# Performance work log

Measured on AMD Instinct MI355X. Metric: run time of the kernel, lower is better.

## Reference

```python
import jax, jax.numpy as jnp
import numpy as np

N = 50000   # nodes
E = 800000  # edges (avg degree 16)
D = 128     # in_dim = out_dim
H = 8       # heads
O = D // H  # per-head dim = 16
FF = 512    # ffn inner hidden
LN_EPS = 1e-6
LRELU_SLOPE = 0.01  # torch F.leaky_relu default


def setup_inputs() -> dict:
    key = jax.random.key(0)
    ks = jax.random.split(key, 9)
    x = jax.random.normal(ks[0], (N, D), jnp.float32)
    src = jax.random.randint(ks[1], (E,), 0, N)
    dst = jax.random.randint(ks[2], (E,), 0, N)
    fc_w = jax.random.normal(ks[3], (H, D, O), jnp.float32) * 0.05
    a_l = jax.random.normal(ks[4], (H, O), jnp.float32) * 0.05
    a_r = jax.random.normal(ks[5], (H, O), jnp.float32) * 0.05
    w1 = jax.random.normal(ks[6], (D, FF), jnp.float32) * 0.05
    b1 = jnp.zeros((FF,), jnp.float32)
    w2 = jax.random.normal(ks[7], (FF, D), jnp.float32) * 0.05
    b2 = jnp.zeros((D,), jnp.float32)
    ln_g = jnp.ones((D,), jnp.float32)
    ln_b = jnp.zeros((D,), jnp.float32)
    return dict(x=x, fc_w=fc_w, a_l=a_l, a_r=a_r, ln_g=ln_g, ln_b=ln_b,
                w1=w1, b1=b1, w2=w2, b2=b2, src=src, dst=dst)


def _gat_s2s(x, fc_w, a_l, a_r, src, dst):
    # per-head projection: [N,H,O]
    z = jnp.einsum('nd,hdo->nho', x, fc_w)
    # attn_fc([z_src||z_dst]) == a_l . z_src + a_r . z_dst  (decomposed, same math)
    el = jnp.einsum('nho,ho->nh', z, a_l)  # [N,H]
    er = jnp.einsum('nho,ho->nh', z, a_r)  # [N,H]
    e = jax.nn.leaky_relu(el[src] + er[dst], LRELU_SLOPE)  # [E,H]
    # edge softmax over incoming edges of each dst node (numerically stable)
    m = jax.ops.segment_max(e, dst, num_segments=N)  # [N,H]
    m = jnp.where(jnp.isfinite(m), m, 0.0)
    ex = jnp.exp(e - m[dst])  # [E,H]
    denom = jax.ops.segment_sum(ex, dst, num_segments=N)  # [N,H]
    alpha = ex / denom[dst]  # [E,H]
    # weighted aggregation of source features: [N,H,O]
    agg = jax.ops.segment_sum(alpha[:, :, None] * z[src], dst, num_segments=N)
    return agg.reshape(N, H * O)  # head concat -> [N,D]


def _ffn(h, ln_g, ln_b, w1, b1, w2, b2):
    # pre-LayerNorm positionwise FFN with gelu and residual (dropout off / eval)
    mu = jnp.mean(h, axis=-1, keepdims=True)
    var = jnp.mean((h - mu) ** 2, axis=-1, keepdims=True)
    ln = (h - mu) * jax.lax.rsqrt(var + LN_EPS) * ln_g + ln_b
    inter = jax.nn.gelu(ln @ w1 + b1, approximate=False)
    return inter @ w2 + b2 + h


def reference(x, fc_w, a_l, a_r, ln_g, ln_b, w1, b1, w2, b2, src, dst):
    h = jax.nn.elu(_gat_s2s(x, fc_w, a_l, a_r, src, dst))
    h = h + x  # residual with origin (S2S: origin == neighbor == x)
    return _ffn(h, ln_g, ln_b, w1, b1, w2, b2)
```

## Files before the change

### kernel.cpp

```cpp
#include <hip/hip_runtime.h>

#define NN 50000
#define EE 800000
#define LDK 136
#define SLOTS 64
#define FEPT 8
#define NFA 157
#define SPLITE (NFA * 256 * FEPT)
#define NFB 234
#define CONVB 2048

#define C_X    0
#define C_ZW   6400000
#define C_AL   6416384
#define C_AR   6416512
#define C_LNG  6416640
#define C_LNB  6416768
#define C_W1T  6416896
#define C_B1   6482432
#define C_W2T  6482944
#define C_B2   6548480
#define C_WAT  6548608
#define C_TOT  6550656

typedef __attribute__((ext_vector_type(8))) short bf16x8;
typedef __attribute__((ext_vector_type(4))) float f32x4;

__device__ __forceinline__ float bf2f(unsigned short u) {
  union { unsigned int i; float f; } v; v.i = ((unsigned int)u) << 16; return v.f;
}
__device__ __forceinline__ unsigned short f2bf(float f) {
  union { float f; unsigned int i; } v; v.f = f;
  unsigned int r = v.i + 0x7fffu + ((v.i >> 16) & 1u);
  return (unsigned short)(r >> 16);
}
__device__ __forceinline__ int ld_idx(const void* p, int i, int is64) {
  return is64 ? (int)((const long long*)p)[i] : ((const int*)p)[i];
}

__device__ __forceinline__ float fast_gelu(float u) {
  float ax = fabsf(u) * 0.70710678118654752f;
  float d  = fmaf(0.3275911f, ax, 1.f);
  float r  = __builtin_amdgcn_rcpf(d);
  r = r * fmaf(-d, r, 2.f);
  float p = fmaf(1.061405429f, r, -1.453152027f);
  p = fmaf(p, r, 1.421413741f);
  p = fmaf(p, r, -0.284496736f);
  p = fmaf(p, r, 0.254829592f);
  p = p * r;
  float e = __expf(-ax * ax);
  float erfv = fmaf(-p, e, 1.f);
  union { float f; unsigned int i; } su, se;
  su.f = u; se.f = erfv;
  se.i = se.i | (su.i & 0x80000000u);
  return 0.5f * u * (1.f + se.f);
}

__global__ void k_probe(const unsigned short* __restrict__ xr,
                        const int* __restrict__ s, const int* __restrict__ d,
                        int* __restrict__ flags) {
  int i = blockIdx.x * 256 + threadIdx.x;
  int bad = 0, zc = 0, zs = 0, zd = 0;
  for (int j = i; j < 65536; j += 32 * 256) {
    unsigned short u = xr[j];
    if ((u & 0x7F80u) == 0x7F80u) bad = 1;
    if (((j & 1) == 0) && u == 0) zc++;
  }
  for (int j = i; j < 131072; j += 32 * 256) {
    if (j & 1) {
      if (s[j] == 0) zs++;
      if (d[j] == 0) zd++;
    }
  }
  if (bad) atomicOr(&flags[0], 1);
  if (zc) atomicAdd(&flags[1], zc);
  if (zs) atomicAdd(&flags[2], zs);
  if (zd) atomicAdd(&flags[3], zd);
}

__device__ __forceinline__ void do_fill(const void* __restrict__ src,
                                        const void* __restrict__ dst,
                                        const int* __restrict__ iflags,
                                        int* __restrict__ cnt,
                                        unsigned short* __restrict__ esrc,
                                        int base) {
  if (base >= EE) return;
  const int s64 = iflags[0] > 1000, d64 = iflags[1] > 1000;
  int dv[FEPT], sv[FEPT];
  if (!d64 && base + FEPT <= EE) {
    const int4* p = (const int4*)((const int*)dst + base);
    int4 a = p[0], b = p[1];
    dv[0]=a.x; dv[1]=a.y; dv[2]=a.z; dv[3]=a.w; dv[4]=b.x; dv[5]=b.y; dv[6]=b.z; dv[7]=b.w;
  } else {
#pragma unroll
    for (int j = 0; j < FEPT; j++) dv[j] = (base + j < EE) ? ld_idx(dst, base + j, d64) : 0;
  }
  if (!s64 && base + FEPT <= EE) {
    const int4* p = (const int4*)((const int*)src + base);
    int4 a = p[0], b = p[1];
    sv[0]=a.x; sv[1]=a.y; sv[2]=a.z; sv[3]=a.w; sv[4]=b.x; sv[5]=b.y; sv[6]=b.z; sv[7]=b.w;
  } else {
#pragma unroll
    for (int j = 0; j < FEPT; j++) sv[j] = (base + j < EE) ? ld_idx(src, base + j, s64) : 0;
  }
#pragma unroll
  for (int j = 0; j < FEPT; j++) {
    if (base + j < EE) {
      unsigned d = (unsigned)dv[j]; if (d >= NN) d = 0;
      unsigned s = (unsigned)sv[j]; if (s >= NN) s = 0;
      int p = atomicAdd(&cnt[d], 1);
      if (p < SLOTS) esrc[d * SLOTS + p] = (unsigned short)s;
    }
  }
}

__global__ __launch_bounds__(256) void k_convfill(
    const void* __restrict__ x, const void* __restrict__ fcw,
    const void* __restrict__ a_l, const void* __restrict__ a_r,
    const void* __restrict__ lng, const void* __restrict__ lnb,
    const void* __restrict__ w1, const void* __restrict__ b1,
    const void* __restrict__ w2, const void* __restrict__ b2,
    const int* __restrict__ flags, unsigned short* __restrict__ canon,
    const void* __restrict__ srcp, const void* __restrict__ dstp,
    int* __restrict__ cnt, unsigned short* __restrict__ esrc) {
  if (blockIdx.x < NFA) {
    do_fill(srcp, dstp, flags + 2, cnt, esrc, (blockIdx.x * 256 + threadIdx.x) * FEPT);
    return;
  }
  const int isf32 = (flags[0] != 0) || (flags[1] > 8192);
  const int tid0 = (blockIdx.x - NFA) * 256 + threadIdx.x;
  for (int v = tid0; v < (C_ZW >> 3); v += CONVB * 256) {
    if (isf32) {
      const float* xf = (const float*)x + v * 8;
      float4 a = *(const float4*)xf;
      float4 b = *(const float4*)(xf + 4);
      union { unsigned short u[8]; uint4 q; } pk;
      pk.u[0] = f2bf(a.x); pk.u[1] = f2bf(a.y); pk.u[2] = f2bf(a.z); pk.u[3] = f2bf(a.w);
      pk.u[4] = f2bf(b.x); pk.u[5] = f2bf(b.y); pk.u[6] = f2bf(b.z); pk.u[7] = f2bf(b.w);
      *(uint4*)(canon + v * 8) = pk.q;
    } else {
      *(uint4*)(canon + v * 8) = *(const uint4*)((const unsigned short*)x + v * 8);
    }
  }
  for (int i = C_ZW + tid0; i < C_TOT; i += CONVB * 256) {
    unsigned short v;
    if (i >= C_WAT) {
      int j = i - C_WAT; int c = j >> 7, dd = j & 127; int h = c & 7;
      const void* fa = (c < 8) ? a_l : a_r;
      float s = 0.f;
      if (isf32) {
        const float* fw = (const float*)fcw + h * 2048 + dd * 16;
        const float* fv = (const float*)fa + h * 16;
#pragma unroll
        for (int o = 0; o < 16; o++) s += fw[o] * fv[o];
      } else {
        const unsigned short* fw = (const unsigned short*)fcw + h * 2048 + dd * 16;
        const unsigned short* fv = (const unsigned short*)fa + h * 16;
#pragma unroll
        for (int o = 0; o < 16; o++) s += bf2f(fw[o]) * bf2f(fv[o]);
      }
      v = f2bf(s);
    } else {
      const void* src; int idx;
      if (i < C_AL)       { int j = i - C_ZW; int c = j >> 7, d = j & 127; src = fcw; idx = (c >> 4) * 2048 + d * 16 + (c & 15); }
      else if (i < C_AR)  { src = a_l; idx = i - C_AL; }
      else if (i < C_LNG) { src = a_r; idx = i - C_AR; }
      else if (i < C_LNB) { src = lng; idx = i - C_LNG; }
      else if (i < C_W1T) { src = lnb; idx = i - C_LNB; }
      else if (i < C_B1)  { int j = i - C_W1T; int n = j >> 7, k = j & 127; src = w1; idx = k * 512 + n; }
      else if (i < C_W2T) { src = b1;  idx = i - C_B1; }
      else if (i < C_B2)  { int j = i - C_W2T; int n = j >> 9, k = j & 511; src = w2; idx = k * 128 + n; }
      else                { src = b2;  idx = i - C_B2; }
      if (isf32) v = f2bf(((const float*)src)[idx]);
      else       v = ((const unsigned short*)src)[idx];
    }
    canon[i] = v;
  }
}

__global__ __launch_bounds__(256) void k_projfill(
    const unsigned short* __restrict__ canon,
    unsigned short* __restrict__ z, float* __restrict__ el, float* __restrict__ er,
    const void* __restrict__ srcp, const void* __restrict__ dstp,
    const int* __restrict__ iflags,
    int* __restrict__ cnt, unsigned short* __restrict__ esrc) {
  __shared__ unsigned short sA[128 * LDK];
  __shared__ unsigned short sB[64 * LDK];
  if (blockIdx.x < NFB) {
    do_fill(srcp, dstp, iflags, cnt, esrc,
            SPLITE + (blockIdx.x * 256 + threadIdx.x) * FEPT);
    return;
  }
  const int pid = blockIdx.x - NFB;
  const unsigned short* xc  = canon + C_X;
  const unsigned short* zwt = canon + C_ZW;
  const unsigned short* wat = canon + C_WAT;
  const int tid = threadIdx.x;
  const int row0 = (pid >> 1) * 128;
  const int n0 = (pid & 1) * 64;
  for (int v = tid; v < 2048; v += 256) {
    int r = v >> 4, k8 = (v & 15) << 3;
    int gr = row0 + r; if (gr >= NN) gr = NN - 1;
    *(uint4*)(&sA[r * LDK + k8]) = *(const uint4*)(xc + gr * 128 + k8);
  }
  for (int v = tid; v < 1024; v += 256) {
    int n = v >> 4, k8 = (v & 15) << 3;
    *(uint4*)(&sB[n * LDK + k8]) = *(const uint4*)(zwt + (n0 + n) * 128 + k8);
  }
  __syncthreads();
  const int lane = tid & 63, w = tid >> 6;
  const int mr = lane & 15, q = lane >> 4;
  const f32x4 zero = {0.f, 0.f, 0.f, 0.f};
  f32x4 acc[8];
#pragma unroll
  for (int i = 0; i < 8; i++) acc[i] = zero;
#pragma unroll
  for (int kc = 0; kc < 4; kc++) {
    bf16x8 b = *(const bf16x8*)(&sB[(w * 16 + mr) * LDK + kc * 32 + q * 8]);
#pragma unroll
    for (int mt = 0; mt < 8; mt++) {
      bf16x8 a = *(const bf16x8*)(&sA[(mt * 16 + mr) * LDK + kc * 32 + q * 8]);
      acc[mt] = __builtin_amdgcn_mfma_f32_16x16x32_bf16(a, b, acc[mt], 0, 0, 0);
    }
  }
  const int col = n0 + w * 16 + mr;
#pragma unroll
  for (int mt = 0; mt < 8; mt++) {
#pragma unroll
    for (int r = 0; r < 4; r++) {
      int grow = row0 + mt * 16 + q * 4 + r;
      if (grow < NN) z[grow * 128 + col] = f2bf(acc[mt][r]);
    }
  }
  if (n0 == 0) {
    f32x4 e0 = zero, e1 = zero;
#pragma unroll
    for (int kc = 0; kc < 4; kc++) {
      bf16x8 b = *(const bf16x8*)(wat + mr * 128 + kc * 32 + q * 8);
      bf16x8 a0 = *(const bf16x8*)(&sA[(w * 16 + mr) * LDK + kc * 32 + q * 8]);
      bf16x8 a1 = *(const bf16x8*)(&sA[((w + 4) * 16 + mr) * LDK + kc * 32 + q * 8]);
      e0 = __builtin_amdgcn_mfma_f32_16x16x32_bf16(a0, b, e0, 0, 0, 0);
      e1 = __builtin_amdgcn_mfma_f32_16x16x32_bf16(a1, b, e1, 0, 0, 0);
    }
    float* eo = (mr < 8) ? el : er;
    const int hh = mr & 7;
#pragma unroll
    for (int r = 0; r < 4; r++) {
      int g0 = row0 + w * 16 + q * 4 + r;
      int g1 = row0 + (w + 4) * 16 + q * 4 + r;
      if (g0 < NN) eo[g0 * 8 + hh] = e0[r];
      if (g1 < NN) eo[g1 * 8 + hh] = e1[r];
    }
  }
}

__global__ __launch_bounds__(256) void k_agg(
    const unsigned short* __restrict__ canon, const unsigned short* __restrict__ z,
    const float* __restrict__ el, const float* __restrict__ er,
    const int* __restrict__ cnt, const unsigned short* __restrict__ esrc,
    const void* __restrict__ srcp, const void* __restrict__ dstp,
    const int* __restrict__ iflags,
    float* __restrict__ h1out, float2* __restrict__ mars) {
  const unsigned short* xc = canon + C_X;
  const int lane = threadIdx.x & 63;
  const int node = blockIdx.x * 4 + (threadIdx.x >> 6);
  if (node >= NN) return;
  const int degr = cnt[node];
  const int hl = lane & 7;
  const int g  = lane >> 3;
  const float ern = er[node * 8 + hl];

  float m = -3.0e38f;
  float acc[16];
#pragma unroll
  for (int j = 0; j < 16; j++) acc[j] = 0.f;
  float denom = 0.f;

  if (degr <= SLOTS) {
    const int deg = degr;
    const unsigned short* eptr = esrc + node * SLOTS;
    for (int b = 0; b < deg; b += 16) {
      int e0 = b + g, e1 = b + g + 8;
      int c0 = (e0 < deg) ? e0 : deg - 1;
      int c1 = (e1 < deg) ? e1 : deg - 1;
      unsigned s0 = eptr[c0]; if (s0 >= NN) s0 = 0;
      unsigned s1 = eptr[c1]; if (s1 >= NN) s1 = 0;
      float t0 = el[s0 * 8 + hl] + ern;
      float t1 = el[s1 * 8 + hl] + ern;
      t0 = (t0 > 0.f) ? t0 : 0.01f * t0;
      t1 = (t1 > 0.f) ? t1 : 0.01f * t1;
      if (e0 < deg) m = fmaxf(m, t0);
      if (e1 < deg) m = fmaxf(m, t1);
    }
    m = fmaxf(m, __shfl_xor(m, 8));
    m = fmaxf(m, __shfl_xor(m, 16));
    m = fmaxf(m, __shfl_xor(m, 32));
    for (int b = 0; b < deg; b += 16) {
      int e0 = b + g, e1 = b + g + 8;
      int c0 = (e0 < deg) ? e0 : deg - 1;
      int c1 = (e1 < deg) ? e1 : deg - 1;
      unsigned s0 = eptr[c0]; if (s0 >= NN) s0 = 0;
      unsigned s1 = eptr[c1]; if (s1 >= NN) s1 = 0;
      float t0 = el[s0 * 8 + hl] + ern;
      float t1 = el[s1 * 8 + hl] + ern;
      bf16x8 za0 = *(const bf16x8*)(z + s0 * 128 + hl * 16);
      bf16x8 za1 = *(const bf16x8*)(z + s0 * 128 + hl * 16 + 8);
      bf16x8 zb0 = *(const bf16x8*)(z + s1 * 128 + hl * 16);
      bf16x8 zb1 = *(const bf16x8*)(z + s1 * 128 + hl * 16 + 8);
      t0 = (t0 > 0.f) ? t0 : 0.01f * t0;
      t1 = (t1 > 0.f) ? t1 : 0.01f * t1;
      float ex0 = (e0 < deg) ? __expf(fminf(t0 - m, 0.f)) : 0.f;
      float ex1 = (e1 < deg) ? __expf(fminf(t1 - m, 0.f)) : 0.f;
      denom += ex0 + ex1;
#pragma unroll
      for (int j = 0; j < 8; j++) {
        acc[j]     += ex0 * bf2f((unsigned short)za0[j]) + ex1 * bf2f((unsigned short)zb0[j]);
        acc[j + 8] += ex0 * bf2f((unsigned short)za1[j]) + ex1 * bf2f((unsigned short)zb1[j]);
      }
    }
  } else {
    const int s64 = iflags[0] > 1000, d64 = iflags[1] > 1000;
    for (int b = 0; b < EE; b += 8) {
      int e = b + g;
      unsigned dd = (unsigned)ld_idx(dstp, e, d64); if (dd >= NN) dd = 0;
      bool ok = (dd == (unsigned)node);
      unsigned s0 = (unsigned)ld_idx(srcp, e, s64); if (s0 >= NN) s0 = 0;
      float t0 = el[s0 * 8 + hl] + ern;
      t0 = (t0 > 0.f) ? t0 : 0.01f * t0;
      if (ok) m = fmaxf(m, t0);
    }
    m = fmaxf(m, __shfl_xor(m, 8));
    m = fmaxf(m, __shfl_xor(m, 16));
    m = fmaxf(m, __shfl_xor(m, 32));
    for (int b = 0; b < EE; b += 8) {
      int e = b + g;
      unsigned dd = (unsigned)ld_idx(dstp, e, d64); if (dd >= NN) dd = 0;
      bool ok = (dd == (unsigned)node);
      unsigned s0 = (unsigned)ld_idx(srcp, e, s64); if (s0 >= NN) s0 = 0;
      float t0 = el[s0 * 8 + hl] + ern;
      t0 = (t0 > 0.f) ? t0 : 0.01f * t0;
      float ex0 = ok ? __expf(fminf(t0 - m, 0.f)) : 0.f;
      denom += ex0;
      bf16x8 za0 = *(const bf16x8*)(z + s0 * 128 + hl * 16);
      bf16x8 za1 = *(const bf16x8*)(z + s0 * 128 + hl * 16 + 8);
#pragma unroll
      for (int j = 0; j < 8; j++) {
        acc[j]     += ex0 * bf2f((unsigned short)za0[j]);
        acc[j + 8] += ex0 * bf2f((unsigned short)za1[j]);
      }
    }
  }

  denom += __shfl_xor(denom, 8);
  denom += __shfl_xor(denom, 16);
  denom += __shfl_xor(denom, 32);
  {
    const bool hi1 = (lane & 32) != 0;
#pragma unroll
    for (int j = 0; j < 8; j++) {
      float send = hi1 ? acc[j] : acc[j + 8];
      float recv = __shfl_xor(send, 32);
      float keep = hi1 ? acc[j + 8] : acc[j];
      acc[j] = keep + recv;
    }
    const bool hi2 = (lane & 16) != 0;
#pragma unroll
    for (int j = 0; j < 4; j++) {
      float send = hi2 ? acc[j] : acc[j + 4];
      float recv = __shfl_xor(send, 16);
      float keep = hi2 ? acc[j + 4] : acc[j];
      acc[j] = keep + recv;
    }
    const bool hi3 = (lane & 8) != 0;
#pragma unroll
    for (int j = 0; j < 2; j++) {
      float send = hi3 ? acc[j] : acc[j + 2];
      float recv = __shfl_xor(send, 8);
      float keep = hi3 ? acc[j + 2] : acc[j];
      acc[j] = keep + recv;
    }
  }
  const float inv = (denom > 0.f) ? 1.f / denom : 0.f;
  const int c = hl * 16 + g * 2;
  float r0 = acc[0] * inv;
  float r1 = acc[1] * inv;
  unsigned int xx = *(const unsigned int*)(xc + node * 128 + c);
  float hv0 = ((r0 > 0.f) ? r0 : (__expf(fminf(r0, 0.f)) - 1.f)) + bf2f((unsigned short)(xx & 0xffffu));
  float hv1 = ((r1 > 0.f) ? r1 : (__expf(fminf(r1, 0.f)) - 1.f)) + bf2f((unsigned short)(xx >> 16));
  float s1 = hv0 + hv1;
  float s2 = hv0 * hv0 + hv1 * hv1;
#pragma unroll
  for (int off = 1; off < 64; off <<= 1) {
    s1 += __shfl_xor(s1, off);
    s2 += __shfl_xor(s2, off);
  }
  if (lane == 0) {
    float mu = s1 * (1.f / 128.f);
    float var = s2 * (1.f / 128.f) - mu * mu;
    mars[node] = make_float2(mu, rsqrtf(fmaxf(var, 0.f) + 1e-6f));
  }
  *(float2*)(h1out + node * 128 + c) = make_float2(hv0, hv1);
}

__global__ __launch_bounds__(512) void k_ffn(
    const unsigned short* __restrict__ canon, const float2* __restrict__ mars,
    float* __restrict__ out) {
  const unsigned short* lngc = canon + C_LNG;
  const unsigned short* lnbc = canon + C_LNB;
  const unsigned short* w1t  = canon + C_W1T;
  const unsigned short* b1c  = canon + C_B1;
  const unsigned short* w2t  = canon + C_W2T;
  const unsigned short* b2c  = canon + C_B2;
  __shared__ unsigned short sLn[64 * LDK];
  __shared__ unsigned short sInt[64 * LDK];
  const int tid = threadIdx.x;
  const int row0 = blockIdx.x * 64;
  {
    const int r = tid >> 3, t8 = tid & 7;
    const int grow = row0 + r;
    const int gr = (grow < NN) ? grow : NN - 1;
    const float2 ms = mars[gr];
    const float* hrow = out + (size_t)gr * 128 + t8 * 16;
#pragma unroll
    for (int h8 = 0; h8 < 2; h8++) {
      float4 a = *(const float4*)(hrow + h8 * 8);
      float4 b = *(const float4*)(hrow + h8 * 8 + 4);
      union { unsigned short u[8]; uint4 q; } gv, bv, pk;
      gv.q = *(const uint4*)(lngc + t8 * 16 + h8 * 8);
      bv.q = *(const uint4*)(lnbc + t8 * 16 + h8 * 8);
      float vv[8] = {a.x, a.y, a.z, a.w, b.x, b.y, b.z, b.w};
#pragma unroll
      for (int j = 0; j < 8; j++)
        pk.u[j] = f2bf((vv[j] - ms.x) * ms.y * bf2f(gv.u[j]) + bf2f(bv.u[j]));
      *(uint4*)(&sLn[r * LDK + t8 * 16 + h8 * 8]) = pk.q;
    }
  }
  __syncthreads();
  const int lane = tid & 63, w = tid >> 6;
  const int mr = lane & 15, q = lane >> 4;
  const f32x4 zero = {0.f, 0.f, 0.f, 0.f};
  f32x4 acc2[4];
#pragma unroll
  for (int a = 0; a < 4; a++) acc2[a] = zero;
#pragma unroll
  for (int qr = 0; qr < 4; qr++) {
    if (qr) __syncthreads();
    const int colg = qr * 128 + w * 16;
    f32x4 a1[4];
#pragma unroll
    for (int a = 0; a < 4; a++) a1[a] = zero;
#pragma unroll
    for (int kc = 0; kc < 4; kc++) {
      bf16x8 wf = *(const bf16x8*)(w1t + (colg + mr) * 128 + kc * 32 + q * 8);
#pragma unroll
      for (int rt = 0; rt < 4; rt++) {
        bf16x8 lf = *(const bf16x8*)(&sLn[(rt * 16 + mr) * LDK + kc * 32 + q * 8]);
        a1[rt] = __builtin_amdgcn_mfma_f32_16x16x32_bf16(wf, lf, a1[rt], 0, 0, 0);
      }
    }
    union { unsigned short u[4]; uint2 v; } b1v;
    b1v.v = *(const uint2*)(b1c + colg + q * 4);
#pragma unroll
    for (int rt = 0; rt < 4; rt++) {
      union { unsigned short u[4]; uint2 v; } pk;
#pragma unroll
      for (int r = 0; r < 4; r++)
        pk.u[r] = f2bf(fast_gelu(a1[rt][r] + bf2f(b1v.u[r])));
      *(uint2*)(&sInt[(rt * 16 + mr) * LDK + w * 16 + q * 4]) = pk.v;
    }
    __syncthreads();
#pragma unroll
    for (int ks = 0; ks < 4; ks++) {
      bf16x8 bw = *(const bf16x8*)(w2t + (w * 16 + mr) * 512 + qr * 128 + ks * 32 + q * 8);
#pragma unroll
      for (int mt = 0; mt < 4; mt++) {
        bf16x8 af = *(const bf16x8*)(&sInt[(mt * 16 + mr) * LDK + ks * 32 + q * 8]);
        acc2[mt] = __builtin_amdgcn_mfma_f32_16x16x32_bf16(af, bw, acc2[mt], 0, 0, 0);
      }
    }
  }
  {
    const int col = w * 16 + mr;
    const float bias = bf2f(b2c[col]);
#pragma unroll
    for (int mt = 0; mt < 4; mt++)
#pragma unroll
      for (int r = 0; r < 4; r++) {
        int grow = row0 + mt * 16 + q * 4 + r;
        if (grow < NN) {
          size_t o = (size_t)grow * 128 + col;
          out[o] = acc2[mt][r] + bias + out[o];
        }
      }
  }
}

extern "C" void kernel_launch(void* const* d_in, const int* in_sizes, int n_in,
                              void* d_out, int out_size, void* d_ws, size_t ws_size,
                              hipStream_t stream) {
  const void* x   = d_in[0];
  const void* fcw = d_in[1];
  const void* a_l = d_in[2];
  const void* a_r = d_in[3];
  const void* lng = d_in[4];
  const void* lnb = d_in[5];
  const void* w1  = d_in[6];
  const void* b1  = d_in[7];
  const void* w2  = d_in[8];
  const void* b2  = d_in[9];
  const void* src = d_in[10];
  const void* dst = d_in[11];
  float* out = (float*)d_out;

  char* ws = (char*)d_ws;
  size_t off = 0;
  auto alloc = [&](size_t bytes) -> char* {
    char* p = ws + off; off += (bytes + 255) & ~(size_t)255; return p;
  };
  int* flags            = (int*)alloc(64);
  int* iflags           = flags + 2;
  int* cnt              = (int*)alloc((size_t)NN * 4);
  unsigned short* esrc  = (unsigned short*)alloc((size_t)NN * SLOTS * 2);
  unsigned short* canon = (unsigned short*)alloc((size_t)C_TOT * 2);
  unsigned short* z     = (unsigned short*)alloc((size_t)NN * 128 * 2);
  float* el             = (float*)alloc((size_t)NN * 8 * 4);
  float* er             = (float*)alloc((size_t)NN * 8 * 4);
  float2* mars          = (float2*)alloc((size_t)NN * 8);

  hipMemsetAsync(ws, 0, 256 + (size_t)NN * 4, stream);
  k_probe<<<32, 256, 0, stream>>>((const unsigned short*)x, (const int*)src, (const int*)dst, flags);
  k_convfill<<<NFA + CONVB, 256, 0, stream>>>(x, fcw, a_l, a_r, lng, lnb, w1, b1, w2, b2,
                                              flags, canon, src, dst, cnt, esrc);
  k_projfill<<<NFB + 391 * 2, 256, 0, stream>>>(canon, z, el, er, src, dst, iflags, cnt, esrc);
  k_agg<<<(NN + 3) / 4, 256, 0, stream>>>(canon, z, el, er, cnt, esrc, src, dst, iflags, out, mars);
  k_ffn<<<(NN + 63) / 64, 512, 0, stream>>>(canon, mars, out);
}
```

Measured before the change: 242.2 us.

## Read raw x directly in projection and aggregation, drop bf16 copy of x, shrink FFN tile

Stops materialising a bf16 copy of x in a separate pass. The projection kernel now converts fp32 x to bf16 while staging into shared memory, and the aggregation residual reads raw x directly. The weight-conversion kernel is shrunk to weights only, and all edge filling moves into the projection launch. The FFN tile drops from 64 to 32 rows per block to raise block count, at the cost of reusing each weight load over fewer rows.

```diff
diff --git a/kernel.cpp b/kernel.cpp
--- a/kernel.cpp
+++ b/kernel.cpp
@@ -5,23 +5,19 @@
 #define LDK 136
 #define SLOTS 64
 #define FEPT 8
-#define NFA 157
-#define SPLITE (NFA * 256 * FEPT)
-#define NFB 234
-#define CONVB 2048
-
-#define C_X    0
-#define C_ZW   6400000
-#define C_AL   6416384
-#define C_AR   6416512
-#define C_LNG  6416640
-#define C_LNB  6416768
-#define C_W1T  6416896
-#define C_B1   6482432
-#define C_W2T  6482944
-#define C_B2   6548480
-#define C_WAT  6548608
-#define C_TOT  6550656
+#define NFB 391
+
+#define C_ZW   0
+#define C_AL   16384
+#define C_AR   16512
+#define C_LNG  16640
+#define C_LNB  16768
+#define C_W1T  16896
+#define C_B1   82432
+#define C_W2T  82944
+#define C_B2   148480
+#define C_WAT  148608
+#define C_TOT  150656
 
 typedef __attribute__((ext_vector_type(8))) short bf16x8;
 typedef __attribute__((ext_vector_type(4))) float f32x4;
@@ -78,6 +74,50 @@
   if (zd) atomicAdd(&flags[3], zd);
 }
 
+__global__ __launch_bounds__(256) void k_convert(
+    const void* __restrict__ fcw,
+    const void* __restrict__ a_l, const void* __restrict__ a_r,
+    const void* __restrict__ lng, const void* __restrict__ lnb,
+    const void* __restrict__ w1, const void* __restrict__ b1,
+    const void* __restrict__ w2, const void* __restrict__ b2,
+    const int* __restrict__ flag, unsigned short* __restrict__ canon) {
+  const int isf32 = (flag[0] != 0) || (flag[1] > 8192);
+  for (int i = blockIdx.x * 256 + threadIdx.x; i < C_TOT; i += gridDim.x * 256) {
+    unsigned short v;
+    if (i >= C_WAT) {
+      int j = i - C_WAT; int c = j >> 7, dd = j & 127; int h = c & 7;
+      const void* fa = (c < 8) ? a_l : a_r;
+      float s = 0.f;
+      if (isf32) {
+        const float* fw = (const float*)fcw + h * 2048 + dd * 16;
+        const float* fv = (const float*)fa + h * 16;
+#pragma unroll
+        for (int o = 0; o < 16; o++) s += fw[o] * fv[o];
+      } else {
+        const unsigned short* fw = (const unsigned short*)fcw + h * 2048 + dd * 16;
+        const unsigned short* fv = (const unsigned short*)fa + h * 16;
+#pragma unroll
+        for (int o = 0; o < 16; o++) s += bf2f(fw[o]) * bf2f(fv[o]);
+      }
+      v = f2bf(s);
+    } else {
+      const void* src; int idx;
+      if (i < C_AL)       { int c = i >> 7, d = i & 127; src = fcw; idx = (c >> 4) * 2048 + d * 16 + (c & 15); }
+      else if (i < C_AR)  { src = a_l; idx = i - C_AL; }
+      else if (i < C_LNG) { src = a_r; idx = i - C_AR; }
+      else if (i < C_LNB) { src = lng; idx = i - C_LNG; }
+      else if (i < C_W1T) { src = lnb; idx = i - C_LNB; }
+      else if (i < C_B1)  { int j = i - C_W1T; int n = j >> 7, k = j & 127; src = w1; idx = k * 512 + n; }
+      else if (i < C_W2T) { src = b1;  idx = i - C_B1; }
+      else if (i < C_B2)  { int j = i - C_W2T; int n = j >> 9, k = j & 511; src = w2; idx = k * 128 + n; }
+      else                { src = b2;  idx = i - C_B2; }
+      if (isf32) v = f2bf(((const float*)src)[idx]);
+      else       v = ((const unsigned short*)src)[idx];
+    }
+    canon[i] = v;
+  }
+}
+
 __device__ __forceinline__ void do_fill(const void* __restrict__ src,
                                         const void* __restrict__ dst,
                                         const int* __restrict__ iflags,
@@ -114,94 +154,39 @@
   }
 }
 
-__global__ __launch_bounds__(256) void k_convfill(
-    const void* __restrict__ x, const void* __restrict__ fcw,
-    const void* __restrict__ a_l, const void* __restrict__ a_r,
-    const void* __restrict__ lng, const void* __restrict__ lnb,
-    const void* __restrict__ w1, const void* __restrict__ b1,
-    const void* __restrict__ w2, const void* __restrict__ b2,
-    const int* __restrict__ flags, unsigned short* __restrict__ canon,
-    const void* __restrict__ srcp, const void* __restrict__ dstp,
-    int* __restrict__ cnt, unsigned short* __restrict__ esrc) {
-  if (blockIdx.x < NFA) {
-    do_fill(srcp, dstp, flags + 2, cnt, esrc, (blockIdx.x * 256 + threadIdx.x) * FEPT);
-    return;
-  }
-  const int isf32 = (flags[0] != 0) || (flags[1] > 8192);
-  const int tid0 = (blockIdx.x - NFA) * 256 + threadIdx.x;
-  for (int v = tid0; v < (C_ZW >> 3); v += CONVB * 256) {
-    if (isf32) {
-      const float* xf = (const float*)x + v * 8;
-      float4 a = *(const float4*)xf;
-      float4 b = *(const float4*)(xf + 4);
-      union { unsigned short u[8]; uint4 q; } pk;
-      pk.u[0] = f2bf(a.x); pk.u[1] = f2bf(a.y); pk.u[2] = f2bf(a.z); pk.u[3] = f2bf(a.w);
-      pk.u[4] = f2bf(b.x); pk.u[5] = f2bf(b.y); pk.u[6] = f2bf(b.z); pk.u[7] = f2bf(b.w);
-      *(uint4*)(canon + v * 8) = pk.q;
-    } else {
-      *(uint4*)(canon + v * 8) = *(const uint4*)((const unsigned short*)x + v * 8);
-    }
-  }
-  for (int i = C_ZW + tid0; i < C_TOT; i += CONVB * 256) {
-    unsigned short v;
-    if (i >= C_WAT) {
-      int j = i - C_WAT; int c = j >> 7, dd = j & 127; int h = c & 7;
-      const void* fa = (c < 8) ? a_l : a_r;
-      float s = 0.f;
-      if (isf32) {
-        const float* fw = (const float*)fcw + h * 2048 + dd * 16;
-        const float* fv = (const float*)fa + h * 16;
-#pragma unroll
-        for (int o = 0; o < 16; o++) s += fw[o] * fv[o];
-      } else {
-        const unsigned short* fw = (const unsigned short*)fcw + h * 2048 + dd * 16;
-        const unsigned short* fv = (const unsigned short*)fa + h * 16;
-#pragma unroll
-        for (int o = 0; o < 16; o++) s += bf2f(fw[o]) * bf2f(fv[o]);
-      }
-      v = f2bf(s);
-    } else {
-      const void* src; int idx;
-      if (i < C_AL)       { int j = i - C_ZW; int c = j >> 7, d = j & 127; src = fcw; idx = (c >> 4) * 2048 + d * 16 + (c & 15); }
-      else if (i < C_AR)  { src = a_l; idx = i - C_AL; }
-      else if (i < C_LNG) { src = a_r; idx = i - C_AR; }
-      else if (i < C_LNB) { src = lng; idx = i - C_LNG; }
-      else if (i < C_W1T) { src = lnb; idx = i - C_LNB; }
-      else if (i < C_B1)  { int j = i - C_W1T; int n = j >> 7, k = j & 127; src = w1; idx = k * 512 + n; }
-      else if (i < C_W2T) { src = b1;  idx = i - C_B1; }
-      else if (i < C_B2)  { int j = i - C_W2T; int n = j >> 9, k = j & 511; src = w2; idx = k * 128 + n; }
-      else                { src = b2;  idx = i - C_B2; }
-      if (isf32) v = f2bf(((const float*)src)[idx]);
-      else       v = ((const unsigned short*)src)[idx];
-    }
-    canon[i] = v;
-  }
-}
-
 __global__ __launch_bounds__(256) void k_projfill(
-    const unsigned short* __restrict__ canon,
+    const unsigned short* __restrict__ canon, const void* __restrict__ xraw,
     unsigned short* __restrict__ z, float* __restrict__ el, float* __restrict__ er,
     const void* __restrict__ srcp, const void* __restrict__ dstp,
-    const int* __restrict__ iflags,
+    const int* __restrict__ flags,
     int* __restrict__ cnt, unsigned short* __restrict__ esrc) {
   __shared__ unsigned short sA[128 * LDK];
   __shared__ unsigned short sB[64 * LDK];
   if (blockIdx.x < NFB) {
-    do_fill(srcp, dstp, iflags, cnt, esrc,
-            SPLITE + (blockIdx.x * 256 + threadIdx.x) * FEPT);
+    do_fill(srcp, dstp, flags + 2, cnt, esrc, (blockIdx.x * 256 + threadIdx.x) * FEPT);
     return;
   }
   const int pid = blockIdx.x - NFB;
-  const unsigned short* xc  = canon + C_X;
   const unsigned short* zwt = canon + C_ZW;
   const unsigned short* wat = canon + C_WAT;
+  const int isf32 = (flags[0] != 0) || (flags[1] > 8192);
   const int tid = threadIdx.x;
   const int row0 = (pid >> 1) * 128;
   const int n0 = (pid & 1) * 64;
   for (int v = tid; v < 2048; v += 256) {
     int r = v >> 4, k8 = (v & 15) << 3;
     int gr = row0 + r; if (gr >= NN) gr = NN - 1;
-    *(uint4*)(&sA[r * LDK + k8]) = *(const uint4*)(xc + gr * 128 + k8);
+    if (isf32) {
+      const float* xf = (const float*)xraw + gr * 128 + k8;
+      float4 a = *(const float4*)xf;
+      float4 b = *(const float4*)(xf + 4);
+      union { unsigned short u[8]; uint4 q; } pk;
+      pk.u[0] = f2bf(a.x); pk.u[1] = f2bf(a.y); pk.u[2] = f2bf(a.z); pk.u[3] = f2bf(a.w);
+      pk.u[4] = f2bf(b.x); pk.u[5] = f2bf(b.y); pk.u[6] = f2bf(b.z); pk.u[7] = f2bf(b.w);
+      *(uint4*)(&sA[r * LDK + k8]) = pk.q;
+    } else {
+      *(uint4*)(&sA[r * LDK + k8]) = *(const uint4*)((const unsigned short*)xraw + gr * 128 + k8);
+    }
   }
   for (int v = tid; v < 1024; v += 256) {
     int n = v >> 4, k8 = (v & 15) << 3;
@@ -255,13 +240,12 @@
 }
 
 __global__ __launch_bounds__(256) void k_agg(
-    const unsigned short* __restrict__ canon, const unsigned short* __restrict__ z,
+    const void* __restrict__ xraw, const unsigned short* __restrict__ z,
     const float* __restrict__ el, const float* __restrict__ er,
     const int* __restrict__ cnt, const unsigned short* __restrict__ esrc,
     const void* __restrict__ srcp, const void* __restrict__ dstp,
-    const int* __restrict__ iflags,
+    const int* __restrict__ flags,
     float* __restrict__ h1out, float2* __restrict__ mars) {
-  const unsigned short* xc = canon + C_X;
   const int lane = threadIdx.x & 63;
   const int node = blockIdx.x * 4 + (threadIdx.x >> 6);
   if (node >= NN) return;
@@ -319,7 +303,7 @@
       }
     }
   } else {
-    const int s64 = iflags[0] > 1000, d64 = iflags[1] > 1000;
+    const int s64 = flags[2] > 1000, d64 = flags[3] > 1000;
     for (int b = 0; b < EE; b += 8) {
       int e = b + g;
       unsigned dd = (unsigned)ld_idx(dstp, e, d64); if (dd >= NN) dd = 0;
@@ -384,9 +368,17 @@
   const int c = hl * 16 + g * 2;
   float r0 = acc[0] * inv;
   float r1 = acc[1] * inv;
-  unsigned int xx = *(const unsigned int*)(xc + node * 128 + c);
-  float hv0 = ((r0 > 0.f) ? r0 : (__expf(fminf(r0, 0.f)) - 1.f)) + bf2f((unsigned short)(xx & 0xffffu));
-  float hv1 = ((r1 > 0.f) ? r1 : (__expf(fminf(r1, 0.f)) - 1.f)) + bf2f((unsigned short)(xx >> 16));
+  float xv0, xv1;
+  if ((flags[0] != 0) || (flags[1] > 8192)) {
+    float2 t = *(const float2*)((const float*)xraw + (size_t)node * 128 + c);
+    xv0 = t.x; xv1 = t.y;
+  } else {
+    unsigned int xx = *(const unsigned int*)((const unsigned short*)xraw + (size_t)node * 128 + c);
+    xv0 = bf2f((unsigned short)(xx & 0xffffu));
+    xv1 = bf2f((unsigned short)(xx >> 16));
+  }
+  float hv0 = ((r0 > 0.f) ? r0 : (__expf(fminf(r0, 0.f)) - 1.f)) + xv0;
+  float hv1 = ((r1 > 0.f) ? r1 : (__expf(fminf(r1, 0.f)) - 1.f)) + xv1;
   float s1 = hv0 + hv1;
   float s2 = hv0 * hv0 + hv1 * hv1;
 #pragma unroll
@@ -411,49 +403,44 @@
   const unsigned short* b1c  = canon + C_B1;
   const unsigned short* w2t  = canon + C_W2T;
   const unsigned short* b2c  = canon + C_B2;
-  __shared__ unsigned short sLn[64 * LDK];
-  __shared__ unsigned short sInt[64 * LDK];
+  __shared__ unsigned short sLn[32 * LDK];
+  __shared__ unsigned short sInt[32 * LDK];
   const int tid = threadIdx.x;
-  const int row0 = blockIdx.x * 64;
+  const int row0 = blockIdx.x * 32;
   {
-    const int r = tid >> 3, t8 = tid & 7;
+    const int r = tid >> 4, t16 = tid & 15;
     const int grow = row0 + r;
     const int gr = (grow < NN) ? grow : NN - 1;
     const float2 ms = mars[gr];
-    const float* hrow = out + (size_t)gr * 128 + t8 * 16;
-#pragma unroll
-    for (int h8 = 0; h8 < 2; h8++) {
-      float4 a = *(const float4*)(hrow + h8 * 8);
-      float4 b = *(const float4*)(hrow + h8 * 8 + 4);
-      union { unsigned short u[8]; uint4 q; } gv, bv, pk;
-      gv.q = *(const uint4*)(lngc + t8 * 16 + h8 * 8);
-      bv.q = *(const uint4*)(lnbc + t8 * 16 + h8 * 8);
-      float vv[8] = {a.x, a.y, a.z, a.w, b.x, b.y, b.z, b.w};
-#pragma unroll
-      for (int j = 0; j < 8; j++)
-        pk.u[j] = f2bf((vv[j] - ms.x) * ms.y * bf2f(gv.u[j]) + bf2f(bv.u[j]));
-      *(uint4*)(&sLn[r * LDK + t8 * 16 + h8 * 8]) = pk.q;
-    }
+    const float* hrow = out + (size_t)gr * 128 + t16 * 8;
+    float4 a = *(const float4*)(hrow);
+    float4 b = *(const float4*)(hrow + 4);
+    union { unsigned short u[8]; uint4 q; } gv, bv, pk;
+    gv.q = *(const uint4*)(lngc + t16 * 8);
+    bv.q = *(const uint4*)(lnbc + t16 * 8);
+    float vv[8] = {a.x, a.y, a.z, a.w, b.x, b.y, b.z, b.w};
+#pragma unroll
+    for (int j = 0; j < 8; j++)
+      pk.u[j] = f2bf((vv[j] - ms.x) * ms.y * bf2f(gv.u[j]) + bf2f(bv.u[j]));
+    *(uint4*)(&sLn[r * LDK + t16 * 8]) = pk.q;
   }
   __syncthreads();
   const int lane = tid & 63, w = tid >> 6;
   const int mr = lane & 15, q = lane >> 4;
   const f32x4 zero = {0.f, 0.f, 0.f, 0.f};
-  f32x4 acc2[4];
-#pragma unroll
-  for (int a = 0; a < 4; a++) acc2[a] = zero;
+  f32x4 acc2[2];
+  acc2[0] = zero; acc2[1] = zero;
 #pragma unroll
   for (int qr = 0; qr < 4; qr++) {
     if (qr) __syncthreads();
     const int colg = qr * 128 + w * 16;
-    f32x4 a1[4];
-#pragma unroll
-    for (int a = 0; a < 4; a++) a1[a] = zero;
+    f32x4 a1[2];
+    a1[0] = zero; a1[1] = zero;
 #pragma unroll
     for (int kc = 0; kc < 4; kc++) {
       bf16x8 wf = *(const bf16x8*)(w1t + (colg + mr) * 128 + kc * 32 + q * 8);
 #pragma unroll
-      for (int rt = 0; rt < 4; rt++) {
+      for (int rt = 0; rt < 2; rt++) {
         bf16x8 lf = *(const bf16x8*)(&sLn[(rt * 16 + mr) * LDK + kc * 32 + q * 8]);
         a1[rt] = __builtin_amdgcn_mfma_f32_16x16x32_bf16(wf, lf, a1[rt], 0, 0, 0);
       }
@@ -461,7 +448,7 @@
     union { unsigned short u[4]; uint2 v; } b1v;
     b1v.v = *(const uint2*)(b1c + colg + q * 4);
 #pragma unroll
-    for (int rt = 0; rt < 4; rt++) {
+    for (int rt = 0; rt < 2; rt++) {
       union { unsigned short u[4]; uint2 v; } pk;
 #pragma unroll
       for (int r = 0; r < 4; r++)
@@ -473,7 +460,7 @@
     for (int ks = 0; ks < 4; ks++) {
       bf16x8 bw = *(const bf16x8*)(w2t + (w * 16 + mr) * 512 + qr * 128 + ks * 32 + q * 8);
 #pragma unroll
-      for (int mt = 0; mt < 4; mt++) {
+      for (int mt = 0; mt < 2; mt++) {
         bf16x8 af = *(const bf16x8*)(&sInt[(mt * 16 + mr) * LDK + ks * 32 + q * 8]);
         acc2[mt] = __builtin_amdgcn_mfma_f32_16x16x32_bf16(af, bw, acc2[mt], 0, 0, 0);
       }
@@ -483,7 +470,7 @@
     const int col = w * 16 + mr;
     const float bias = bf2f(b2c[col]);
 #pragma unroll
-    for (int mt = 0; mt < 4; mt++)
+    for (int mt = 0; mt < 2; mt++)
 #pragma unroll
       for (int r = 0; r < 4; r++) {
         int grow = row0 + mt * 16 + q * 4 + r;
@@ -518,7 +505,6 @@
     char* p = ws + off; off += (bytes + 255) & ~(size_t)255; return p;
   };
   int* flags            = (int*)alloc(64);
-  int* iflags           = flags + 2;
   int* cnt              = (int*)alloc((size_t)NN * 4);
   unsigned short* esrc  = (unsigned short*)alloc((size_t)NN * SLOTS * 2);
   unsigned short* canon = (unsigned short*)alloc((size_t)C_TOT * 2);
@@ -529,9 +515,8 @@
 
   hipMemsetAsync(ws, 0, 256 + (size_t)NN * 4, stream);
   k_probe<<<32, 256, 0, stream>>>((const unsigned short*)x, (const int*)src, (const int*)dst, flags);
-  k_convfill<<<NFA + CONVB, 256, 0, stream>>>(x, fcw, a_l, a_r, lng, lnb, w1, b1, w2, b2,
-                                              flags, canon, src, dst, cnt, esrc);
-  k_projfill<<<NFB + 391 * 2, 256, 0, stream>>>(canon, z, el, er, src, dst, iflags, cnt, esrc);
-  k_agg<<<(NN + 3) / 4, 256, 0, stream>>>(canon, z, el, er, cnt, esrc, src, dst, iflags, out, mars);
-  k_ffn<<<(NN + 63) / 64, 512, 0, stream>>>(canon, mars, out);
-}
+  k_convert<<<256, 256, 0, stream>>>(fcw, a_l, a_r, lng, lnb, w1, b1, w2, b2, flags, canon);
+  k_projfill<<<NFB + 391 * 2, 256, 0, stream>>>(canon, x, z, el, er, src, dst, flags, cnt, esrc);
+  k_agg<<<(NN + 3) / 4, 256, 0, stream>>>(x, z, el, er, cnt, esrc, src, dst, flags, out, mars);
+  k_ffn<<<(NN + 31) / 32, 512, 0, stream>>>(canon, mars, out);
+}
```

Result: slower. 261.1 us (+7.8%).
